# Kernel optimization log

Measured on AMD Instinct MI355X. Metric: run time of the kernel, lower is better.

Reference implementation:

```python
import jax, jax.numpy as jnp
import numpy as np

DIM, H, HD = 1024, 16, 64

def setup_inputs() -> dict:
    key = jax.random.key(0)
    ks = jax.random.split(key, 9)
    s = 1.0 / np.sqrt(DIM)
    return {
        "x": jax.random.normal(ks[0], (4, 4096, DIM), dtype=jnp.float32),
        "time_mix": jnp.ones((1, 1, DIM), dtype=jnp.float32),
        "time_decay": jnp.ones((H, HD), dtype=jnp.float32),
        "time_first": jnp.zeros((H, HD), dtype=jnp.float32),
        "Wk": jax.random.uniform(ks[1], (DIM, DIM), jnp.float32, -s, s),
        "Wv": jax.random.uniform(ks[2], (DIM, DIM), jnp.float32, -s, s),
        "Wr": jax.random.uniform(ks[3], (DIM, DIM), jnp.float32, -s, s),
        "Wg": jax.random.uniform(ks[4], (DIM, DIM), jnp.float32, -s, s),
        "Wo": jax.random.uniform(ks[5], (DIM, DIM), jnp.float32, -s, s),
    }

def reference(x, time_mix, time_decay, time_first, Wk, Wv, Wr, Wg, Wo):
    B, T, D = x.shape
    xx = time_mix * x
    # torch Linear: y = x @ W.T
    def proj(W):
        return jnp.einsum('btd,ed->bte', xx, W).reshape(B, T, H, HD)
    k = proj(Wk)
    v = proj(Wv)
    r = proj(Wr)
    g = jax.nn.silu(proj(Wg))
    decay = jnp.exp(-time_decay)[None, :, :, None]        # [1,H,K,1]
    tf = time_first[None]                                  # [1,H,K]
    state0 = jnp.zeros((B, H, HD, HD), dtype=x.dtype)      # [B,H,K,V]

    def step(state, inp):
        k_t, v_t, r_t, g_t = inp                           # each [B,H,K]
        state = state * decay + k_t[..., :, None] * v_t[..., None, :]
        wkv = jnp.einsum('bhkv,bhk->bhv', state, k_t) + tf * k_t * v_t
        return state, r_t * wkv * g_t

    # time-major for scan: [T,B,H,K]
    tm = lambda a: jnp.moveaxis(a, 1, 0)
    state, outs = jax.lax.scan(step, state0, (tm(k), tm(v), tm(r), tm(g)))
    out = jnp.moveaxis(outs, 0, 1).reshape(B, T, D)        # [B,T,D]
    out = jnp.einsum('btd,ed->bte', out, Wo)
    return out, state
```

## Files before the change

### kernel.cpp

```cpp
#include <hip/hip_runtime.h>
#include <stdint.h>

#define DIM 1024
#define NH  16
#define HD  64
#define BB  4
#define TT  4096
#define BT  (BB*TT)
#define NC  32
#define CL  128

typedef __bf16 bf16x8 __attribute__((ext_vector_type(8)));
typedef float  f32x4  __attribute__((ext_vector_type(4)));

__device__ __forceinline__ float bfu(unsigned int u) {
    return __uint_as_float((u & 0xffffu) << 16);
}
__device__ __forceinline__ unsigned short f2bf(float f) {
    unsigned int u = __float_as_uint(f);
    u += 0x7fffu + ((u >> 16) & 1u);
    return (unsigned short)(u >> 16);
}

__device__ __forceinline__ void gload16(const void* g, void* lds) {
    __builtin_amdgcn_global_load_lds((__attribute__((address_space(1))) void*)g,
                                     (__attribute__((address_space(3))) void*)lds,
                                     16, 0, 0);
}


__global__ __launch_bounds__(256) void conv_x_kernel(
    const float* __restrict__ x, const float* __restrict__ tmix,
    unsigned short* __restrict__ xx)
{
    int gid = blockIdx.x * 256 + threadIdx.x;
    float4 xv = ((const float4*)x)[gid];
    float4 tv = ((const float4*)tmix)[gid & 255];
    uint2 o;
    o.x = (unsigned)f2bf(xv.x * tv.x) | ((unsigned)f2bf(xv.y * tv.y) << 16);
    o.y = (unsigned)f2bf(xv.z * tv.z) | ((unsigned)f2bf(xv.w * tv.w) << 16);
    ((uint2*)xx)[gid] = o;
}

__global__ __launch_bounds__(256) void conv_w_kernel(
    const float* __restrict__ Wk, const float* __restrict__ Wv,
    const float* __restrict__ Wr, const float* __restrict__ Wg,
    const float* __restrict__ Wo,
    unsigned short* __restrict__ wcat, unsigned short* __restrict__ wob)
{
    int gid = blockIdx.x * 256 + threadIdx.x;
    size_t idx = (size_t)gid * 4;
    float4 v;
    unsigned short* dst;
    if (idx < 4194304) {
        int p = (int)(idx >> 20);
        size_t loc = idx & 1048575;
        const float* src = (p == 0) ? Wk : (p == 1) ? Wv : (p == 2) ? Wr : Wg;
        v = ((const float4*)src)[loc >> 2];
        dst = wcat + idx;
    } else {
        size_t loc = idx - 4194304;
        v = ((const float4*)Wo)[loc >> 2];
        dst = wob + loc;
    }
    uint2 o;
    o.x = (unsigned)f2bf(v.x) | ((unsigned)f2bf(v.y) << 16);
    o.y = (unsigned)f2bf(v.z) | ((unsigned)f2bf(v.w) << 16);
    *(uint2*)dst = o;
}


#define MFMAQ(accb, av, bv)                                                    \
    _Pragma("unroll") for (int mi_ = 0; mi_ < 4; ++mi_)                        \
    _Pragma("unroll") for (int ni_ = 0; ni_ < 4; ++ni_)                        \
        acc[(accb)+mi_][ni_] = __builtin_amdgcn_mfma_f32_16x16x32_bf16(        \
            av[mi_], bv[ni_], acc[(accb)+mi_][ni_], 0, 0, 0);

#define LDA4(dst, mib, kh, bi)                                                 \
    _Pragma("unroll") for (int q_ = 0; q_ < 4; ++q_)                           \
        dst[q_] = *(const bf16x8*)&As[bi][(kh)*8192 + (arow + ((mib)+q_)*16)*32 + kxu];

#define LDB4(dst, kh, bi)                                                      \
    _Pragma("unroll") for (int q_ = 0; q_ < 4; ++q_)                           \
        dst[q_] = *(const bf16x8*)&Bs[bi][(kh)*8192 + (brow + q_*16)*32 + kxu];

#define STAGE_A(nb, kh, k0e) do {                                              \
    gload16(Asrc0 + (k0e) + (kh)*32, &As[nb][(kh)*8192 + d0]);                 \
    gload16(Asrc1 + (k0e) + (kh)*32, &As[nb][(kh)*8192 + d1]); } while (0)

#define STAGE_B(nb, kh, k0e) do {                                              \
    gload16(Bsrc0 + (k0e) + (kh)*32, &Bs[nb][(kh)*8192 + d0]);                 \
    gload16(Bsrc1 + (k0e) + (kh)*32, &Bs[nb][(kh)*8192 + d1]); } while (0)

#define SBAR()  __builtin_amdgcn_s_barrier()
#define SCHED0() __builtin_amdgcn_sched_barrier(0)
#define WAIT_LGKM0() asm volatile("s_waitcnt lgkmcnt(0)" ::: "memory")
#define WAIT_VM(n)   asm volatile("s_waitcnt vmcnt(" #n ")" ::: "memory")

template<int EPI>
__global__ __launch_bounds__(512, 2) void gemm256(
    const unsigned short* __restrict__ A, const unsigned short* __restrict__ B,
    float* __restrict__ C, int M, int N, int K,
    unsigned short* __restrict__ kb, unsigned short* __restrict__ vb,
    unsigned short* __restrict__ rb, unsigned short* __restrict__ gb)
{
    __shared__ unsigned short As[2][16384];
    __shared__ unsigned short Bs[2][16384];

    const int tid  = threadIdx.x;
    const int lane = tid & 63;
    const int wv   = tid >> 6;
    const int wr   = wv >> 2;
    const int wc   = wv & 3;
    const int lrow = lane & 15;
    const int kseg = lane >> 4;

    const int nwg = gridDim.x;
    const int cpx = nwg >> 3;
    const int bid = blockIdx.x;
    const int wg  = (bid & 7) * cpx + (bid >> 3);
    const int nbx = N >> 8;
    const int bx = wg % nbx, by = wg / nbx;
    const size_t bm = (size_t)by * 256, bn = (size_t)bx * 256;

    const int r0 = tid >> 2;
    const int c0 = (tid & 3) ^ (((tid >> 5) & 1) << 1);
    const int r1 = (512 + tid) >> 2;
    const int c1 = (tid & 3) ^ ((((512 + tid) >> 5) & 1) << 1);
    const unsigned short* Asrc0 = A + (bm + r0) * (size_t)K + c0 * 8;
    const unsigned short* Asrc1 = A + (bm + r1) * (size_t)K + c1 * 8;
    const unsigned short* Bsrc0 = B + (bn + r0) * (size_t)K + c0 * 8;
    const unsigned short* Bsrc1 = B + (bn + r1) * (size_t)K + c1 * 8;
    const int d0 = (tid & 448) * 8;
    const int d1 = (512 + (tid & 448)) * 8;

    const int arow = wr * 128 + lrow;
    const int brow = wc * 64 + lrow;
    const int kxu  = ((kseg * 16) ^ ((lrow >> 3) << 5)) >> 1;

    f32x4 acc[8][4] = {};
    bf16x8 aP[4], aQ[4], bP[4], bQ[4];
    const int NT = K >> 6;

    STAGE_A(0, 0, 0); STAGE_B(0, 0, 0); STAGE_A(0, 1, 0); STAGE_B(0, 1, 0);
    WAIT_VM(4);
    SBAR(); SCHED0();
    LDA4(aP, 0, 0, 0);
    LDB4(bP, 0, 0);
    SCHED0();

    for (int t = 0; t < NT; ++t) {
        const int bufc = t & 1, bufn = bufc ^ 1;
        const int k0n = (t + 1) << 6;
        const bool more = (t + 1 < NT);
        SBAR();
        WAIT_LGKM0(); SCHED0();
        if (more) STAGE_A(bufn, 0, k0n);
        __builtin_amdgcn_s_setprio(1);
        MFMAQ(0, aP, bP);
        __builtin_amdgcn_s_setprio(0);
        LDA4(aQ, 4, 0, bufc);
        SCHED0();
        WAIT_VM(2);
        SBAR();
        WAIT_LGKM0(); SCHED0();
        if (more) STAGE_B(bufn, 0, k0n);
        __builtin_amdgcn_s_setprio(1);
        MFMAQ(4, aQ, bP);
        __builtin_amdgcn_s_setprio(0);
        LDA4(aP, 0, 1, bufc);
        LDB4(bQ, 1, bufc);
        SCHED0();
        SBAR();
        WAIT_LGKM0(); SCHED0();
        if (more) STAGE_A(bufn, 1, k0n);
        __builtin_amdgcn_s_setprio(1);
        MFMAQ(0, aP, bQ);
        __builtin_amdgcn_s_setprio(0);
        LDA4(aQ, 4, 1, bufc);
        SCHED0();
        WAIT_VM(2);
        SBAR();
        WAIT_LGKM0(); SCHED0();
        if (more) STAGE_B(bufn, 1, k0n);
        __builtin_amdgcn_s_setprio(1);
        MFMAQ(4, aQ, bQ);
        __builtin_amdgcn_s_setprio(0);
        if (more) {
            LDA4(aP, 0, 0, bufn);
            LDB4(bP, 0, bufn);
        }
        SCHED0();
    }

    if (EPI == 0) {
        const int p = (int)(bn >> 10);
        unsigned short* dst = (p == 0) ? kb : (p == 1) ? vb : (p == 2) ? rb : gb;
        #pragma unroll
        for (int mi = 0; mi < 8; ++mi) {
            const int mbase = (int)bm + wr * 128 + mi * 16 + kseg * 4;
            #pragma unroll
            for (int ni = 0; ni < 4; ++ni) {
                const int n = (int)bn + wc * 64 + ni * 16 + lrow;
                const int e = n & 1023;
                const int h = e >> 6, j = e & 63;
                #pragma unroll
                for (int ri = 0; ri < 4; ++ri) {
                    const int m = mbase + ri;
                    const int b = m >> 12, tt = m & 4095;
                    float v = acc[mi][ni][ri];
                    if (p == 3) v = v / (1.f + __expf(-v));
                    dst[(((size_t)(b * NH + h)) * TT + tt) * HD + j] = f2bf(v);
                }
            }
        }
    } else {
        #pragma unroll
        for (int mi = 0; mi < 8; ++mi) {
            const int mbase = (int)bm + wr * 128 + mi * 16 + kseg * 4;
            #pragma unroll
            for (int ni = 0; ni < 4; ++ni) {
                const int n = (int)bn + wc * 64 + ni * 16 + lrow;
                #pragma unroll
                for (int ri = 0; ri < 4; ++ri)
                    C[(size_t)(mbase + ri) * N + n] = acc[mi][ni][ri];
            }
        }
    }
}


__global__ __launch_bounds__(256) void chunk_fused(
    const unsigned short* __restrict__ kb, const unsigned short* vb,
    const unsigned short* __restrict__ rb, const unsigned short* __restrict__ gb,
    const float* __restrict__ td, const float* __restrict__ tf,
    unsigned short* ctru, unsigned short* __restrict__ outp)
{
    __shared__ unsigned short KS [128 * 64];
    __shared__ unsigned short VT [64 * 128];
    __shared__ unsigned short Qm [32 * 64];
    __shared__ unsigned short QDm[32 * 64];
    __shared__ unsigned short KTB[32 * 64];
    __shared__ unsigned short KDT[64 * 32];
    __shared__ unsigned short PMt[32 * 32];
    __shared__ unsigned short SPT[64 * 64];

    const int bid  = blockIdx.x;
    const int c    = bid & (NC - 1);
    const int bh   = bid >> 5;
    const int h    = bh & (NH - 1);
    const int batch= bh >> 4;
    const int tid  = threadIdx.x;
    const int lane = tid & 63;
    const int w    = tid >> 6;
    const int lrow = lane & 15;
    const int kseg = lane >> 4;

    const float* tdh = td + h * HD;

    const unsigned short* kg_ = kb + ((size_t)bh * TT + (size_t)c * CL) * HD;
    const unsigned short* vg_ = vb + ((size_t)bh * TT + (size_t)c * CL) * HD;
    ((uint4*)KS)[tid]       = ((const uint4*)kg_)[tid];
    ((uint4*)KS)[tid + 256] = ((const uint4*)kg_)[tid + 256];
    ((uint4*)KS)[tid + 512] = ((const uint4*)kg_)[tid + 512];
    ((uint4*)KS)[tid + 768] = ((const uint4*)kg_)[tid + 768];
    #pragma unroll
    for (int it = 0; it < 4; ++it) {
        int ci = it * 256 + tid;
        uint4 r = ((const uint4*)vg_)[ci];
        int s = ci >> 3, j0 = (ci & 7) * 8;
        unsigned int vals[4] = { r.x, r.y, r.z, r.w };
        #pragma unroll
        for (int q = 0; q < 4; ++q) {
            int j1 = j0 + 2 * q, j2 = j1 + 1;
            *(unsigned short*)((char*)VT + ((j1 * 256 + s * 2) ^ ((j1 & 15) << 4)))
                = (unsigned short)(vals[q] & 0xffffu);
            *(unsigned short*)((char*)VT + ((j2 * 256 + s * 2) ^ ((j2 & 15) << 4)))
                = (unsigned short)(vals[q] >> 16);
        }
    }

    const int kkc = tid & 63;
    const float t1 = tdh[kkc];

    float e32[4];
    #pragma unroll
    for (int q = 0; q < 4; ++q)
        e32[q] = __expf(-32.f * tdh[16 * w + kseg * 4 + q]);

    const int it = w >> 1;
    const int st = w & 1;
    const int jt0 = (w & 1) * 2;

    f32x4 acc_S[4] = {};

    for (int sb = 0; sb < 4; ++sb) {
        const int s0 = sb * 32;
        __syncthreads();
        #pragma unroll
        for (int i8 = 0; i8 < 8; ++i8) {
            int r = i8 * 4 + w;
            float kf  = bfu(KS[(s0 + r) * 64 + kkc]);
            float eq  = __expf(-t1 * (float)r);
            float eq1 = __expf(-t1 * (float)(r + 1));
            float ek  = __expf( t1 * (float)r);
            float ekd = __expf(-t1 * (float)(31 - r));
            int rb2 = (r * 128 + kkc * 2) ^ ((r & 7) << 4);
            *(unsigned short*)((char*)Qm  + rb2) = f2bf(kf * eq);
            *(unsigned short*)((char*)QDm + rb2) = f2bf(kf * eq1);
            *(unsigned short*)((char*)KTB + rb2) = f2bf(kf * ek);
            *(unsigned short*)((char*)KDT + ((kkc * 64 + r * 2) ^ ((kkc & 3) << 4)))
                = f2bf(kf * ekd);
        }
        __syncthreads();
        {
            bf16x8 qa[2], kbf[2];
            #pragma unroll
            for (int ks = 0; ks < 2; ++ks) {
                qa[ks] = *(const bf16x8*)((const char*)Qm +
                    (it * 16 + lrow) * 128 + ((kseg * 16 + ks * 64) ^ ((lrow & 7) << 4)));
                kbf[ks] = *(const bf16x8*)((const char*)KTB +
                    (st * 16 + lrow) * 128 + ((kseg * 16 + ks * 64) ^ ((lrow & 7) << 4)));
            }
            f32x4 accP = {};
            accP = __builtin_amdgcn_mfma_f32_16x16x32_bf16(qa[0], kbf[0], accP, 0, 0, 0);
            accP = __builtin_amdgcn_mfma_f32_16x16x32_bf16(qa[1], kbf[1], accP, 0, 0, 0);
            #pragma unroll
            for (int q = 0; q < 4; ++q) {
                int i_ = it * 16 + kseg * 4 + q;
                int s_ = st * 16 + lrow;
                unsigned short pv = (s_ <= i_) ? f2bf(accP[q]) : (unsigned short)0;
                *(unsigned short*)((char*)PMt + ((i_ * 64 + s_ * 2) ^ ((i_ & 3) << 4))) = pv;
            }
        }
        {
            bf16x8 sa = *(const bf16x8*)((const char*)KDT +
                (16 * w + lrow) * 64 + ((kseg * 16) ^ ((lrow & 3) << 4)));
            #pragma unroll
            for (int jt = 0; jt < 4; ++jt) {
                #pragma unroll
                for (int q = 0; q < 4; ++q) acc_S[jt][q] *= e32[q];
                bf16x8 vbf = *(const bf16x8*)((const char*)VT +
                    (jt * 16 + lrow) * 256 + ((s0 * 2 + kseg * 16) ^ ((lrow & 15) << 4)));
                acc_S[jt] = __builtin_amdgcn_mfma_f32_16x16x32_bf16(sa, vbf, acc_S[jt], 0, 0, 0);
            }
        }
        __syncthreads();
        {
            bf16x8 pa = *(const bf16x8*)((const char*)PMt +
                (it * 16 + lrow) * 64 + ((kseg * 16) ^ ((lrow & 3) << 4)));
            bf16x8 qd[2];
            #pragma unroll
            for (int ks = 0; ks < 2; ++ks)
                qd[ks] = *(const bf16x8*)((const char*)QDm +
                    (it * 16 + lrow) * 128 + ((kseg * 16 + ks * 64) ^ ((lrow & 7) << 4)));
            #pragma unroll
            for (int jj = 0; jj < 2; ++jj) {
                const int jt = jt0 + jj;
                const int j_ = jt * 16 + lrow;
                bf16x8 vbf = *(const bf16x8*)((const char*)VT +
                    j_ * 256 + ((s0 * 2 + kseg * 16) ^ ((lrow & 15) << 4)));
                f32x4 accO = {};
                accO = __builtin_amdgcn_mfma_f32_16x16x32_bf16(pa, vbf, accO, 0, 0, 0);
                if (sb > 0) {
                    #pragma unroll
                    for (int ks = 0; ks < 2; ++ks) {
                        bf16x8 sp = *(const bf16x8*)((const char*)SPT +
                            j_ * 128 + ((kseg * 16 + ks * 64) ^ ((lrow & 7) << 4)));
                        accO = __builtin_amdgcn_mfma_f32_16x16x32_bf16(qd[ks], sp, accO, 0, 0, 0);
                    }
                }
                const float tfj = tf[h * HD + j_];
                #pragma unroll
                for (int q = 0; q < 4; ++q) {
                    int ip = it * 16 + kseg * 4 + q;
                    int t_ = c * CL + s0 + ip;
                    float kval = bfu(KS[(s0 + ip) * 64 + j_]);
                    float vval = bfu(*(const unsigned short*)((const char*)VT +
                        j_ * 256 + (((s0 + ip) * 2) ^ ((j_ & 15) << 4))));
                    float val = accO[q] + tfj * kval * vval;
                    size_t e = ((size_t)bh * TT + t_) * HD + j_;
                    float rgv = bfu(rb[e]) * bfu(gb[e]);
                    outp[((size_t)batch * TT + t_) * DIM + h * HD + j_] = f2bf(val * rgv);
                }
            }
        }
        __syncthreads();
        if (sb < 3) {
            #pragma unroll
            for (int jt = 0; jt < 4; ++jt) {
                const int j_ = jt * 16 + lrow;
                #pragma unroll
                for (int q = 0; q < 4; ++q) {
                    int kk_ = 16 * w + kseg * 4 + q;
                    *(unsigned short*)((char*)SPT +
                        ((j_ * 128 + kk_ * 2) ^ ((j_ & 7) << 4))) = f2bf(acc_S[jt][q]);
                }
            }
        }
    }

    unsigned short* cb = ctru + (size_t)bid * 8192;
    #pragma unroll
    for (int jt = 0; jt < 4; ++jt) {
        const int j_ = jt * 16 + lrow;
        uint2 pk;
        pk.x = (unsigned)f2bf(acc_S[jt][0]) | ((unsigned)f2bf(acc_S[jt][1]) << 16);
        pk.y = (unsigned)f2bf(acc_S[jt][2]) | ((unsigned)f2bf(acc_S[jt][3]) << 16);
        *(uint2*)&cb[j_ * 64 + 16 * w + kseg * 4] = pk;
    }
}


__global__ __launch_bounds__(256) void chunk_scan(
    unsigned short* ctru, const float* __restrict__ td,
    float* __restrict__ state_out)
{
    int gtid = blockIdx.x * 256 + threadIdx.x;
    int kk = gtid & 63;
    int j  = (gtid >> 6) & 63;
    int bh = gtid >> 12;
    int h  = bh & (NH - 1);
    float dC = __expf(-(float)CL * td[h * HD + kk]);
    float S = 0.f;
    unsigned short* cs = ctru + (size_t)bh * NC * 8192 + j * 64 + kk;
    for (int c = 0; c < NC; c++) {
        float t = bfu(cs[(size_t)c * 8192]);
        cs[(size_t)c * 8192] = f2bf(S);
        S = __builtin_fmaf(dC, S, t);
    }
    state_out[(size_t)bh * 4096 + kk * 64 + j] = S;
}


__global__ __launch_bounds__(256) void chunk_corr(
    const unsigned short* __restrict__ kb, const unsigned short* __restrict__ rb,
    const unsigned short* __restrict__ gb,
    const float* __restrict__ td, const unsigned short* s0t,
    unsigned short* __restrict__ outp)
{
    const int bid = blockIdx.x;
    const int c   = bid & (NC - 1);
    const int bh  = bid >> 5;
    const int h   = bh & (NH - 1);
    const int b   = bh >> 4;
    const int tid = threadIdx.x;
    const int lane = tid & 63;
    const int w    = tid >> 6;

    __shared__ unsigned short kd[CL * HD];

    const int srow = tid >> 3;
    const int kk0  = (tid & 7) * 8;
    float tdv[8];
    #pragma unroll
    for (int e = 0; e < 8; e++) tdv[e] = td[h * HD + kk0 + e];
    const unsigned short* kbase = kb + ((size_t)bh * TT + (size_t)c * CL) * HD;
    #pragma unroll
    for (int it = 0; it < 4; it++) {
        const int row = it * 32 + srow;
        uint4 r = *(const uint4*)(kbase + (size_t)row * HD + kk0);
        const float fi = -(float)(row + 1);
        unsigned int rr[4] = { r.x, r.y, r.z, r.w };
        unsigned int o[4];
        #pragma unroll
        for (int q = 0; q < 4; q++) {
            float lo = bfu(rr[q])       * __expf(fi * tdv[2*q]);
            float hi = bfu(rr[q] >> 16) * __expf(fi * tdv[2*q+1]);
            o[q] = (unsigned)f2bf(lo) | ((unsigned)f2bf(hi) << 16);
        }
        *(uint4*)((char*)kd + row * 128 + ((kk0 * 2) ^ ((row & 7) << 4))) =
            make_uint4(o[0], o[1], o[2], o[3]);
    }
    __syncthreads();

    const int lrow = lane & 15;
    const int g    = lane >> 4;

    bf16x8 afr[2][4], bfr[2][2];
    const unsigned short* sbase = s0t + (size_t)bid * 8192;
    #pragma unroll
    for (int ks = 0; ks < 2; ks++)
        #pragma unroll
        for (int vt = 0; vt < 4; vt++)
            afr[ks][vt] = *(const bf16x8*)(sbase + (vt * 16 + lrow) * 64 + g * 8 + ks * 32);
    #pragma unroll
    for (int ks = 0; ks < 2; ks++)
        #pragma unroll
        for (int bt = 0; bt < 2; bt++) {
            const int row = w * 32 + bt * 16 + lrow;
            bfr[ks][bt] = *(const bf16x8*)((const char*)kd + row * 128 +
                (((g * 8 + ks * 32) * 2) ^ ((row & 7) << 4)));
        }

    f32x4 acc[4][2] = {};
    #pragma unroll
    for (int ks = 0; ks < 2; ks++)
        #pragma unroll
        for (int vt = 0; vt < 4; vt++)
            #pragma unroll
            for (int bt = 0; bt < 2; bt++)
                acc[vt][bt] = __builtin_amdgcn_mfma_f32_16x16x32_bf16(
                    afr[ks][vt], bfr[ks][bt], acc[vt][bt], 0, 0, 0);

    #pragma unroll
    for (int bt = 0; bt < 2; bt++) {
        const int i = w * 32 + bt * 16 + lrow;
        const size_t t = (size_t)c * CL + i;
        const unsigned short* rrow2 = rb + ((size_t)bh * TT + t) * HD;
        const unsigned short* grow2 = gb + ((size_t)bh * TT + t) * HD;
        unsigned short* orow = outp + ((size_t)b * TT + t) * DIM + h * HD;
        #pragma unroll
        for (int vt = 0; vt < 4; vt++)
            #pragma unroll
            for (int ri = 0; ri < 4; ri++) {
                const int v = vt * 16 + 4 * g + ri;
                float val = bfu(orow[v]) +
                            bfu(rrow2[v]) * bfu(grow2[v]) * acc[vt][bt][ri];
                orow[v] = f2bf(val);
            }
    }
}


static const size_t OFF_XX   = 0;
static const size_t OFF_WCAT = 33554432;
static const size_t OFF_WO   = 41943040;
static const size_t OFF_K    = 44040192;
static const size_t OFF_V    = 77594624;
static const size_t OFF_R    = 111149056;
static const size_t OFF_G    = 144703488;
static const size_t OFF_OP   = 0;

extern "C" void kernel_launch(void* const* d_in, const int* in_sizes, int n_in,
                              void* d_out, int out_size, void* d_ws, size_t ws_size,
                              hipStream_t stream) {
    const float* x   = (const float*)d_in[0];
    const float* tmx = (const float*)d_in[1];
    const float* td  = (const float*)d_in[2];
    const float* tf  = (const float*)d_in[3];
    const float* Wk  = (const float*)d_in[4];
    const float* Wv  = (const float*)d_in[5];
    const float* Wr  = (const float*)d_in[6];
    const float* Wg  = (const float*)d_in[7];
    const float* Wo  = (const float*)d_in[8];

    char* ws = (char*)d_ws;
    unsigned short* xx   = (unsigned short*)(ws + OFF_XX);
    unsigned short* wcat = (unsigned short*)(ws + OFF_WCAT);
    unsigned short* wob  = (unsigned short*)(ws + OFF_WO);
    unsigned short* kb   = (unsigned short*)(ws + OFF_K);
    unsigned short* vb   = (unsigned short*)(ws + OFF_V);
    unsigned short* rb   = (unsigned short*)(ws + OFF_R);
    unsigned short* gb   = (unsigned short*)(ws + OFF_G);
    unsigned short* ctru = (unsigned short*)(ws + OFF_V);
    unsigned short* outp = (unsigned short*)(ws + OFF_OP);

    float* out       = (float*)d_out;
    float* state_out = out + (size_t)BT * DIM;

    conv_x_kernel<<<16384, 256, 0, stream>>>(x, tmx, xx);
    conv_w_kernel<<<5120, 256, 0, stream>>>(Wk, Wv, Wr, Wg, Wo, wcat, wob);
    gemm256<0><<<1024, 512, 0, stream>>>(xx, wcat, nullptr,
                                         BT, 4096, 1024, kb, vb, rb, gb);
    chunk_fused<<<64 * NC, 256, 0, stream>>>(kb, vb, rb, gb, td, tf, ctru, outp);
    chunk_scan<<<1024, 256, 0, stream>>>(ctru, td, state_out);
    chunk_corr<<<64 * NC, 256, 0, stream>>>(kb, rb, gb, td, ctru, outp);
    gemm256<1><<<256, 512, 0, stream>>>(outp, wob, out,
                                        BT, 1024, 1024,
                                        nullptr, nullptr, nullptr, nullptr);
}
```

Measured before the change: 320.1 us.

## Shrink GEMM tiles to 128x128 with 4 waves and simplified double-buffer pipeline

Replaces the 256x256, 8-wave GEMM with a 128x128, 4-wave version that uses half the LDS and issues all eight global loads for the next k-tile at once, with two MFMA phases per iteration instead of four. This creates four times as many workgroups and allows more per CU, which should help load balance and occupancy, especially for the output projection that previously had only 256 blocks. In exchange each tile reuses loaded data less, so global and L2 traffic per FLOP roughly doubles. The added full vmcnt(0) wait at the top of each iteration may also expose more load latency.

Result: slower. 341.4 us (+6.7%).

```diff
diff --git a/kernel.cpp b/kernel.cpp
--- a/kernel.cpp
+++ b/kernel.cpp
@@ -70,48 +70,50 @@
 }
 
 
-#define MFMAQ(accb, av, bv)                                                    \
-    _Pragma("unroll") for (int mi_ = 0; mi_ < 4; ++mi_)                        \
-    _Pragma("unroll") for (int ni_ = 0; ni_ < 4; ++ni_)                        \
-        acc[(accb)+mi_][ni_] = __builtin_amdgcn_mfma_f32_16x16x32_bf16(        \
-            av[mi_], bv[ni_], acc[(accb)+mi_][ni_], 0, 0, 0);
-
-#define LDA4(dst, mib, kh, bi)                                                 \
-    _Pragma("unroll") for (int q_ = 0; q_ < 4; ++q_)                           \
-        dst[q_] = *(const bf16x8*)&As[bi][(kh)*8192 + (arow + ((mib)+q_)*16)*32 + kxu];
-
-#define LDB4(dst, kh, bi)                                                      \
-    _Pragma("unroll") for (int q_ = 0; q_ < 4; ++q_)                           \
-        dst[q_] = *(const bf16x8*)&Bs[bi][(kh)*8192 + (brow + q_*16)*32 + kxu];
-
-#define STAGE_A(nb, kh, k0e) do {                                              \
-    gload16(Asrc0 + (k0e) + (kh)*32, &As[nb][(kh)*8192 + d0]);                 \
-    gload16(Asrc1 + (k0e) + (kh)*32, &As[nb][(kh)*8192 + d1]); } while (0)
-
-#define STAGE_B(nb, kh, k0e) do {                                              \
-    gload16(Bsrc0 + (k0e) + (kh)*32, &Bs[nb][(kh)*8192 + d0]);                 \
-    gload16(Bsrc1 + (k0e) + (kh)*32, &Bs[nb][(kh)*8192 + d1]); } while (0)
-
 #define SBAR()  __builtin_amdgcn_s_barrier()
 #define SCHED0() __builtin_amdgcn_sched_barrier(0)
 #define WAIT_LGKM0() asm volatile("s_waitcnt lgkmcnt(0)" ::: "memory")
 #define WAIT_VM(n)   asm volatile("s_waitcnt vmcnt(" #n ")" ::: "memory")
 
+#define MFMAQ16(av, bv)                                                        \
+    _Pragma("unroll") for (int mi_ = 0; mi_ < 4; ++mi_)                        \
+    _Pragma("unroll") for (int ni_ = 0; ni_ < 4; ++ni_)                        \
+        acc[mi_][ni_] = __builtin_amdgcn_mfma_f32_16x16x32_bf16(               \
+            av[mi_], bv[ni_], acc[mi_][ni_], 0, 0, 0);
+
+#define LDA4k(dst, kh, bi)                                                     \
+    _Pragma("unroll") for (int q_ = 0; q_ < 4; ++q_)                           \
+        dst[q_] = *(const bf16x8*)&As[bi][(kh)*4096 + (arow + q_*16)*32 + kxu];
+
+#define LDB4k(dst, kh, bi)                                                     \
+    _Pragma("unroll") for (int q_ = 0; q_ < 4; ++q_)                           \
+        dst[q_] = *(const bf16x8*)&Bs[bi][(kh)*4096 + (brow + q_*16)*32 + kxu];
+
+#define STAGE8(nb, k0e) do {                                                   \
+    gload16(Asrc0 + (k0e),      &As[nb][d0]);                                  \
+    gload16(Asrc1 + (k0e),      &As[nb][2048 + d0]);                           \
+    gload16(Bsrc0 + (k0e),      &Bs[nb][d0]);                                  \
+    gload16(Bsrc1 + (k0e),      &Bs[nb][2048 + d0]);                           \
+    gload16(Asrc0 + (k0e) + 32, &As[nb][4096 + d0]);                           \
+    gload16(Asrc1 + (k0e) + 32, &As[nb][4096 + 2048 + d0]);                    \
+    gload16(Bsrc0 + (k0e) + 32, &Bs[nb][4096 + d0]);                           \
+    gload16(Bsrc1 + (k0e) + 32, &Bs[nb][4096 + 2048 + d0]); } while (0)
+
 template<int EPI>
-__global__ __launch_bounds__(512, 2) void gemm256(
+__global__ __launch_bounds__(256, 2) void gemm128(
     const unsigned short* __restrict__ A, const unsigned short* __restrict__ B,
     float* __restrict__ C, int M, int N, int K,
     unsigned short* __restrict__ kb, unsigned short* __restrict__ vb,
     unsigned short* __restrict__ rb, unsigned short* __restrict__ gb)
 {
-    __shared__ unsigned short As[2][16384];
-    __shared__ unsigned short Bs[2][16384];
+    __shared__ unsigned short As[2][8192];
+    __shared__ unsigned short Bs[2][8192];
 
     const int tid  = threadIdx.x;
     const int lane = tid & 63;
     const int wv   = tid >> 6;
-    const int wr   = wv >> 2;
-    const int wc   = wv & 3;
+    const int wr   = wv >> 1;
+    const int wc   = wv & 1;
     const int lrow = lane & 15;
     const int kseg = lane >> 4;
 
@@ -119,76 +121,56 @@
     const int cpx = nwg >> 3;
     const int bid = blockIdx.x;
     const int wg  = (bid & 7) * cpx + (bid >> 3);
-    const int nbx = N >> 8;
+    const int nbx = N >> 7;
     const int bx = wg % nbx, by = wg / nbx;
-    const size_t bm = (size_t)by * 256, bn = (size_t)bx * 256;
+    const size_t bm = (size_t)by * 128, bn = (size_t)bx * 128;
 
     const int r0 = tid >> 2;
     const int c0 = (tid & 3) ^ (((tid >> 5) & 1) << 1);
-    const int r1 = (512 + tid) >> 2;
-    const int c1 = (tid & 3) ^ ((((512 + tid) >> 5) & 1) << 1);
     const unsigned short* Asrc0 = A + (bm + r0) * (size_t)K + c0 * 8;
-    const unsigned short* Asrc1 = A + (bm + r1) * (size_t)K + c1 * 8;
+    const unsigned short* Asrc1 = A + (bm + 64 + r0) * (size_t)K + c0 * 8;
     const unsigned short* Bsrc0 = B + (bn + r0) * (size_t)K + c0 * 8;
-    const unsigned short* Bsrc1 = B + (bn + r1) * (size_t)K + c1 * 8;
-    const int d0 = (tid & 448) * 8;
-    const int d1 = (512 + (tid & 448)) * 8;
-
-    const int arow = wr * 128 + lrow;
+    const unsigned short* Bsrc1 = B + (bn + 64 + r0) * (size_t)K + c0 * 8;
+    const int d0 = (tid & 192) * 8;
+
+    const int arow = wr * 64 + lrow;
     const int brow = wc * 64 + lrow;
     const int kxu  = ((kseg * 16) ^ ((lrow >> 3) << 5)) >> 1;
 
-    f32x4 acc[8][4] = {};
+    f32x4 acc[4][4] = {};
     bf16x8 aP[4], aQ[4], bP[4], bQ[4];
     const int NT = K >> 6;
 
-    STAGE_A(0, 0, 0); STAGE_B(0, 0, 0); STAGE_A(0, 1, 0); STAGE_B(0, 1, 0);
+    STAGE8(0, 0);
     WAIT_VM(4);
     SBAR(); SCHED0();
-    LDA4(aP, 0, 0, 0);
-    LDB4(bP, 0, 0);
+    LDA4k(aP, 0, 0);
+    LDB4k(bP, 0, 0);
     SCHED0();
 
     for (int t = 0; t < NT; ++t) {
         const int bufc = t & 1, bufn = bufc ^ 1;
         const int k0n = (t + 1) << 6;
         const bool more = (t + 1 < NT);
+        WAIT_VM(0);
         SBAR();
         WAIT_LGKM0(); SCHED0();
-        if (more) STAGE_A(bufn, 0, k0n);
+        if (more) STAGE8(bufn, k0n);
         __builtin_amdgcn_s_setprio(1);
-        MFMAQ(0, aP, bP);
+        MFMAQ16(aP, bP);
         __builtin_amdgcn_s_setprio(0);
-        LDA4(aQ, 4, 0, bufc);
+        LDA4k(aQ, 1, bufc);
+        LDB4k(bQ, 1, bufc);
         SCHED0();
-        WAIT_VM(2);
+        if (more) WAIT_VM(4);
         SBAR();
         WAIT_LGKM0(); SCHED0();
-        if (more) STAGE_B(bufn, 0, k0n);
         __builtin_amdgcn_s_setprio(1);
-        MFMAQ(4, aQ, bP);
-        __builtin_amdgcn_s_setprio(0);
-        LDA4(aP, 0, 1, bufc);
-        LDB4(bQ, 1, bufc);
-        SCHED0();
-        SBAR();
-        WAIT_LGKM0(); SCHED0();
-        if (more) STAGE_A(bufn, 1, k0n);
-        __builtin_amdgcn_s_setprio(1);
-        MFMAQ(0, aP, bQ);
-        __builtin_amdgcn_s_setprio(0);
-        LDA4(aQ, 4, 1, bufc);
-        SCHED0();
-        WAIT_VM(2);
-        SBAR();
-        WAIT_LGKM0(); SCHED0();
-        if (more) STAGE_B(bufn, 1, k0n);
-        __builtin_amdgcn_s_setprio(1);
-        MFMAQ(4, aQ, bQ);
+        MFMAQ16(aQ, bQ);
         __builtin_amdgcn_s_setprio(0);
         if (more) {
-            LDA4(aP, 0, 0, bufn);
-            LDB4(bP, 0, bufn);
+            LDA4k(aP, 0, bufn);
+            LDB4k(bP, 0, bufn);
         }
         SCHED0();
     }
@@ -197,8 +179,8 @@
         const int p = (int)(bn >> 10);
         unsigned short* dst = (p == 0) ? kb : (p == 1) ? vb : (p == 2) ? rb : gb;
         #pragma unroll
-        for (int mi = 0; mi < 8; ++mi) {
-            const int mbase = (int)bm + wr * 128 + mi * 16 + kseg * 4;
+        for (int mi = 0; mi < 4; ++mi) {
+            const int mbase = (int)bm + wr * 64 + mi * 16 + kseg * 4;
             #pragma unroll
             for (int ni = 0; ni < 4; ++ni) {
                 const int n = (int)bn + wc * 64 + ni * 16 + lrow;
@@ -216,8 +198,8 @@
         }
     } else {
         #pragma unroll
-        for (int mi = 0; mi < 8; ++mi) {
-            const int mbase = (int)bm + wr * 128 + mi * 16 + kseg * 4;
+        for (int mi = 0; mi < 4; ++mi) {
+            const int mbase = (int)bm + wr * 64 + mi * 16 + kseg * 4;
             #pragma unroll
             for (int ni = 0; ni < 4; ++ni) {
                 const int n = (int)bn + wc * 64 + ni * 16 + lrow;
@@ -561,12 +543,12 @@
 
     conv_x_kernel<<<16384, 256, 0, stream>>>(x, tmx, xx);
     conv_w_kernel<<<5120, 256, 0, stream>>>(Wk, Wv, Wr, Wg, Wo, wcat, wob);
-    gemm256<0><<<1024, 512, 0, stream>>>(xx, wcat, nullptr,
+    gemm128<0><<<4096, 256, 0, stream>>>(xx, wcat, nullptr,
                                          BT, 4096, 1024, kb, vb, rb, gb);
     chunk_fused<<<64 * NC, 256, 0, stream>>>(kb, vb, rb, gb, td, tf, ctru, outp);
     chunk_scan<<<1024, 256, 0, stream>>>(ctru, td, state_out);
     chunk_corr<<<64 * NC, 256, 0, stream>>>(kb, rb, gb, td, ctru, outp);
-    gemm256<1><<<256, 512, 0, stream>>>(outp, wob, out,
-                                        BT, 1024, 1024,
-                                        nullptr, nullptr, nullptr, nullptr);
-}
+    gemm128<1><<<1024, 256, 0, stream>>>(outp, wob, out,
+                                         BT, 1024, 1024,
+                                         nullptr, nullptr, nullptr, nullptr);
+}
```
